# Kernel optimization log

Hardware: AMD Instinct MI355X
Metric: run time of the kernel (lower is better)

Reference implementation:

```python
import jax, jax.numpy as jnp
import numpy as np

B, N, C = 8, 8192, 256
H, D, S = 8, 32, 32          # heads, dim_head, slice_num
HID = 4 * C                  # mlp hidden


def layernorm(x, w, b, eps=1e-5):
    mu = jnp.mean(x, axis=-1, keepdims=True)
    var = jnp.mean(jnp.square(x - mu), axis=-1, keepdims=True)
    return (x - mu) * jax.lax.rsqrt(var + eps) * w + b


def setup_inputs() -> dict:
    key = jax.random.key(0)
    ks = jax.random.split(key, 16)
    s = lambda fan: 1.0 / np.sqrt(fan)
    return {
        "fx": jax.random.normal(ks[0], (B, N, C), jnp.float32),
        "ln1_w": jnp.ones((C,), jnp.float32),
        "ln1_b": jnp.zeros((C,), jnp.float32),
        "Wx": jax.random.uniform(ks[1], (C, C), jnp.float32, -s(C), s(C)),   # in_project_x weight [inner,dim]
        "bx": jax.random.uniform(ks[2], (C,), jnp.float32, -s(C), s(C)),
        "Wq": jax.random.uniform(ks[3], (S, D), jnp.float32, -s(D), s(D)),
        "Wk": jax.random.uniform(ks[4], (S, D), jnp.float32, -s(D), s(D)),
        "Wv": jax.random.uniform(ks[5], (D, D), jnp.float32, -s(D), s(D)),
        "Wo": jax.random.uniform(ks[6], (C, C), jnp.float32, -s(C), s(C)),   # to_out weight [dim,inner]
        "bo": jax.random.uniform(ks[7], (C,), jnp.float32, -s(C), s(C)),
        "ln2_w": jnp.ones((C,), jnp.float32),
        "ln2_b": jnp.zeros((C,), jnp.float32),
        "W1": jax.random.uniform(ks[8], (HID, C), jnp.float32, -s(C), s(C)),
        "b1": jax.random.uniform(ks[9], (HID,), jnp.float32, -s(C), s(C)),
        "W2": jax.random.uniform(ks[10], (C, HID), jnp.float32, -s(HID), s(HID)),
        "b2": jax.random.uniform(ks[11], (C,), jnp.float32, -s(HID), s(HID)),
    }


def linear_no_attn(x, Wx, bx, Wq, Wk, Wv, Wo, bo):
    # x: [B,N,C]
    x_mid = x @ Wx.T + bx                                   # [B,N,C]
    x_mid = x_mid.reshape(x.shape[0], x.shape[1], H, D).transpose(0, 2, 1, 3)  # [B,H,N,D]
    q = jax.nn.softmax(x_mid @ Wq.T, axis=-1)               # [B,H,N,S], softmax over slices
    k = jax.nn.softmax(x_mid @ Wk.T, axis=-2)               # [B,H,N,S], softmax over tokens
    v = x_mid @ Wv.T                                        # [B,H,N,D]
    kv = jnp.einsum('bhns,bhnd->bhsd', k, v)                # [B,H,S,D]
    qkv = jnp.einsum('bhns,bhsd->bhnd', q, kv)              # [B,H,N,D]
    qkv = qkv.transpose(0, 2, 1, 3).reshape(x.shape[0], x.shape[1], H * D)
    return qkv @ Wo.T + bo


def reference(fx, ln1_w, ln1_b, Wx, bx, Wq, Wk, Wv, Wo, bo, ln2_w, ln2_b, W1, b1, W2, b2):
    h = linear_no_attn(layernorm(fx, ln1_w, ln1_b), Wx, bx, Wq, Wk, Wv, Wo, bo) + fx
    y = layernorm(h, ln2_w, ln2_b)
    y = jax.nn.gelu(y @ W1.T + b1, approximate=False)       # MLP: pre + exact GELU, n_layers=0
    y = y @ W2.T + b2
    return y + h
```

## Files before the change

### kernel.cpp

```cpp
#include <hip/hip_runtime.h>
#include <math.h>


typedef __attribute__((ext_vector_type(8))) short bf8;
typedef __attribute__((ext_vector_type(4))) float f32x4;
typedef __attribute__((ext_vector_type(4))) unsigned short u16x4;
typedef __attribute__((ext_vector_type(8))) unsigned short u16x8;

__device__ __forceinline__ float b2f(unsigned short x) {
  union { unsigned u; float f; } t; t.u = ((unsigned)x) << 16; return t.f;
}
__device__ __forceinline__ unsigned short f2b(float f) {
  union { float f; unsigned u; } t; t.f = f;
  unsigned r = t.u + 0x7fffu + ((t.u >> 16) & 1u);
  return (unsigned short)(r >> 16);
}
__device__ __forceinline__ float gelu_exact(float x) {
  return 0.5f * x * (1.0f + erff(x * 0.7071067811865475f));
}
__device__ __forceinline__ float erf_fast(float x) {
  float ax = fabsf(x);
  float t = __builtin_amdgcn_rcpf(fmaf(0.3275911f, ax, 1.0f));
  float p = t * fmaf(t, fmaf(t, fmaf(t, fmaf(t, 1.061405429f, -1.453152027f),
                                     1.421413741f), -0.284496736f), 0.254829592f);
  float r = 1.0f - p * __expf(-ax * ax);
  return copysignf(r, x);
}
__device__ __forceinline__ float gelu_fast(float x) {
  return 0.5f * x * (1.0f + erf_fast(x * 0.7071067811865475f));
}

typedef __attribute__((address_space(1))) const void gas_void;
typedef __attribute__((address_space(3))) void las_void;
__device__ __forceinline__ void gl_lds16(const void* g, void* l) {
  __builtin_amdgcn_global_load_lds((gas_void*)g, (las_void*)l, 16, 0, 0);
}

__global__ void sniff_kernel(const unsigned* __restrict__ fx, int* __restrict__ flag,
                             unsigned* __restrict__ gate) {
  if (threadIdx.x == 0) {
    int cnt = 0;
    for (int i = 0; i < 64; i++) {
      unsigned e = (fx[i] >> 7) & 0xFFu;
      cnt += (e >= 117u && e <= 130u) ? 1 : 0;
    }
    *flag = (cnt >= 32) ? 1 : 0;
    *gate = 0u;
  }
}

struct CvtDesc { const void* src[15]; int off[15]; int n[15]; };

__global__ __launch_bounds__(256) void cvt_tab(CvtDesc d, unsigned short* __restrict__ wtab,
                                               const int* __restrict__ flagp) {
  const int seg = blockIdx.y;
  const int i = blockIdx.x * 256 + threadIdx.x;
  if (i >= d.n[seg]) return;
  unsigned short o;
  if (*flagp) o = ((const unsigned short*)d.src[seg])[i];
  else        o = f2b(((const float*)d.src[seg])[i]);
  wtab[d.off[seg] + i] = o;
}

__global__ __launch_bounds__(256) void build_big(
    const unsigned short* __restrict__ wq, const unsigned short* __restrict__ wk,
    unsigned short* __restrict__ Wqbig, unsigned short* __restrict__ Wkbig)
{
  const int idx = blockIdx.x * 256 + threadIdx.x;
  const int row = idx >> 8, col = idx & 255;
  const bool same = (row >> 5) == (col >> 5);
  const int wi = (row & 31) * 32 + (col & 31);
  Wqbig[idx] = same ? wq[wi] : (unsigned short)0;
  Wkbig[idx] = same ? wk[wi] : (unsigned short)0;
}

__global__ __launch_bounds__(256) void zero_u16(unsigned short* __restrict__ p, int n) {
  int i8 = (blockIdx.x * 256 + threadIdx.x) * 8;
  if (i8 < n) { u16x8 z = {}; *(u16x8*)&p[i8] = z; }
}

__global__ __launch_bounds__(256) void ln_stats(
    const void* __restrict__ X, const int* __restrict__ flagp, int amode,
    float* __restrict__ MU, float* __restrict__ RS)
{
  const int lane = threadIdx.x & 63;
  const int wave = threadIdx.x >> 6;
  const size_t row = (size_t)blockIdx.x * 4 + wave;
  const size_t base = row * 256 + lane * 4;
  const bool abf = amode ? ((*flagp) != 0) : true;
  float x0, x1, x2, x3;
  if (abf) {
    u16x4 uv = *(const u16x4*)&((const unsigned short*)X)[base];
    x0 = b2f(uv[0]); x1 = b2f(uv[1]); x2 = b2f(uv[2]); x3 = b2f(uv[3]);
  } else {
    f32x4 t = *(const f32x4*)&((const float*)X)[base];
    x0 = t[0]; x1 = t[1]; x2 = t[2]; x3 = t[3];
  }
  float s = x0 + x1 + x2 + x3;
  float q = x0*x0 + x1*x1 + x2*x2 + x3*x3;
  #pragma unroll
  for (int m = 1; m < 64; m <<= 1) { s += __shfl_xor(s, m, 64); q += __shfl_xor(q, m, 64); }
  float mean = s * (1.0f / 256.0f);
  float var  = q * (1.0f / 256.0f) - mean * mean;
  if (lane == 0) { MU[row] = mean; RS[row] = rsqrtf(var + 1e-5f); }
}

__global__ __launch_bounds__(256) void gemm_bt(
    const unsigned short* __restrict__ A,
    const unsigned short* __restrict__ W,
    const unsigned short* __restrict__ bias,
    const void* __restrict__ Res, const int* __restrict__ flagp,
    unsigned short* __restrict__ Y,
    int N, int K, int act, int mz, long wz)
{
  __shared__ __align__(16) unsigned short smem[3 * 8192];
  const int tid = threadIdx.x, lane = tid & 63, wave = tid >> 6;
  const size_t zrow = (size_t)blockIdx.z * mz;
  const int bm = blockIdx.x * 128, bn = blockIdx.y * 128;
  const int wm = (wave >> 1) * 64, wn = (wave & 1) * 64;
  const int quad = lane >> 4, l16 = lane & 15;
  const unsigned short* Wz = W + (size_t)blockIdx.z * wz;

  f32x4 acc[4][4] = {};
  const int r0 = tid >> 2;
  const int co = (tid & 3) * 8;
  const unsigned short* pa0 = &A[(zrow + bm + r0) * K + co];
  const unsigned short* pa1 = &A[(zrow + bm + r0 + 64) * K + co];
  const unsigned short* pb0 = &Wz[(size_t)(bn + r0) * K + co];
  const unsigned short* pb1 = &Wz[(size_t)(bn + r0 + 64) * K + co];
  const int nt = K >> 5;

  auto stage = [&](int t, int sl) {
    const int k0 = t << 5;
    unsigned short* b_ = &smem[sl * 8192 + tid * 8];
    gl_lds16(pa0 + k0, b_);
    gl_lds16(pa1 + k0, b_ + 2048);
    gl_lds16(pb0 + k0, b_ + 4096);
    gl_lds16(pb1 + k0, b_ + 6144);
  };

  stage(0, 0);
  if (nt > 1) stage(1, 1);
  int scur = 0, snew = 2;
  for (int t = 0; t < nt; ++t) {
    if (t + 2 < nt) {
      stage(t + 2, snew);
      asm volatile("s_waitcnt vmcnt(8)" ::: "memory");
    } else if (t + 1 < nt) {
      asm volatile("s_waitcnt vmcnt(4)" ::: "memory");
    } else {
      asm volatile("s_waitcnt vmcnt(0)" ::: "memory");
    }
    __builtin_amdgcn_s_barrier();
    __builtin_amdgcn_sched_barrier(0);

    const unsigned short* sa = &smem[scur * 8192];
    const unsigned short* sb = sa + 4096;
    bf8 af[4], bfr[4];
    #pragma unroll
    for (int i = 0; i < 4; i++) af[i]  = *(const bf8*)&sa[(wm + i * 16 + l16) * 32 + quad * 8];
    #pragma unroll
    for (int j = 0; j < 4; j++) bfr[j] = *(const bf8*)&sb[(wn + j * 16 + l16) * 32 + quad * 8];
    #pragma unroll
    for (int i = 0; i < 4; i++)
      #pragma unroll
      for (int j = 0; j < 4; j++)
        acc[i][j] = __builtin_amdgcn_mfma_f32_16x16x32_bf16(af[i], bfr[j], acc[i][j], 0, 0, 0);

    __builtin_amdgcn_sched_barrier(0);
    __builtin_amdgcn_s_barrier();
    scur = scur + 1 < 3 ? scur + 1 : 0;
    snew = snew + 1 < 3 ? snew + 1 : 0;
  }

  const bool rbf = Res ? ((*flagp) != 0) : true;
  float bv[4];
  #pragma unroll
  for (int j = 0; j < 4; j++) bv[j] = b2f(bias[bn + wn + j * 16 + l16]);
  #pragma unroll
  for (int i = 0; i < 4; i++)
    #pragma unroll
    for (int j = 0; j < 4; j++)
      #pragma unroll
      for (int r = 0; r < 4; r++) {
        float v = acc[i][j][r] + bv[j];
        if (act == 2) v = __expf(v);
        acc[i][j][r] = v;
      }
  if (act == 3) {
    #pragma unroll
    for (int i = 0; i < 4; i++)
      #pragma unroll
      for (int g = 0; g < 2; g++)
        #pragma unroll
        for (int r = 0; r < 4; r++) {
          float a0 = acc[i][2*g][r], a1 = acc[i][2*g+1][r];
          float m = fmaxf(a0, a1);
          #pragma unroll
          for (int msk = 1; msk < 16; msk <<= 1) m = fmaxf(m, __shfl_xor(m, msk, 64));
          float e0 = __expf(a0 - m), e1 = __expf(a1 - m);
          float s = e0 + e1;
          #pragma unroll
          for (int msk = 1; msk < 16; msk <<= 1) s += __shfl_xor(s, msk, 64);
          const float rz = 1.0f / s;
          acc[i][2*g][r] = e0 * rz; acc[i][2*g+1][r] = e1 * rz;
        }
  }

  float* cf = (float*)smem;
  const int whalf = wm >> 6;
  #pragma unroll
  for (int half = 0; half < 2; ++half) {
    __builtin_amdgcn_s_barrier();
    if (whalf == half) {
      #pragma unroll
      for (int i = 0; i < 4; i++)
        #pragma unroll
        for (int j = 0; j < 4; j++)
          #pragma unroll
          for (int r = 0; r < 4; r++)
            cf[(i * 16 + quad * 4 + r) * 132 + wn + j * 16 + l16] = acc[i][j][r];
    }
    __builtin_amdgcn_s_barrier();
    #pragma unroll
    for (int st = 0; st < 4; ++st) {
      const int e = st * 2048 + tid * 8;
      const int row = e >> 7;
      const int col = e & 127;
      const size_t gbase = (zrow + bm + half * 64 + row) * (size_t)N + bn + col;
      float v[8];
      #pragma unroll
      for (int u = 0; u < 8; u++) v[u] = cf[row * 132 + col + u];
      if (Res) {
        if (rbf) {
          u16x8 rv = *(const u16x8*)&((const unsigned short*)Res)[gbase];
          #pragma unroll
          for (int u = 0; u < 8; u++) v[u] += b2f(rv[u]);
        } else {
          f32x4 ra = *(const f32x4*)&((const float*)Res)[gbase];
          f32x4 rb = *(const f32x4*)&((const float*)Res)[gbase + 4];
          v[0] += ra[0]; v[1] += ra[1]; v[2] += ra[2]; v[3] += ra[3];
          v[4] += rb[0]; v[5] += rb[1]; v[6] += rb[2]; v[7] += rb[3];
        }
      }
      u16x8 o;
      #pragma unroll
      for (int u = 0; u < 8; u++) o[u] = f2b(v[u]);
      *(u16x8*)&Y[gbase] = o;
    }
  }
}

__global__ __launch_bounds__(256) void gemm_bt_ln(
    const void* __restrict__ A, const int* __restrict__ flagp, int amode,
    const float* __restrict__ MU, const float* __restrict__ RS,
    const unsigned short* __restrict__ lw, const unsigned short* __restrict__ lb,
    const unsigned short* __restrict__ W, const unsigned short* __restrict__ bias,
    unsigned short* __restrict__ Y, int N, int K, int act)
{
  __shared__ __align__(16) unsigned char smemc[32768];
  unsigned short* lA = (unsigned short*)smemc;
  unsigned short* lB = lA + 4096;
  const int tid = threadIdx.x, lane = tid & 63, wave = tid >> 6;
  const int bm = blockIdx.x * 128, bn = blockIdx.y * 128;
  const int wm = (wave >> 1) * 64, wn = (wave & 1) * 64;
  const int quad = lane >> 4, l16 = lane & 15;
  const bool abf = amode ? ((*flagp) != 0) : true;
  const unsigned short* Ab = (const unsigned short*)A;
  const float* Af = (const float*)A;

  f32x4 acc[4][4] = {};
  const int r0 = tid >> 2;
  const int co = (tid & 3) * 8;
  const unsigned short* pb0 = &W[(size_t)(bn + r0) * K + co];
  const unsigned short* pb1 = &W[(size_t)(bn + r0 + 64) * K + co];

  for (int k0 = 0; k0 < K; k0 += 32) {
    u16x8 wv8 = *(const u16x8*)&lw[k0 + co];
    u16x8 bv8 = *(const u16x8*)&lb[k0 + co];
    __syncthreads();
    gl_lds16(pb0 + k0, &lB[tid * 8]);
    gl_lds16(pb1 + k0, &lB[2048 + tid * 8]);
    #pragma unroll
    for (int half = 0; half < 2; half++) {
      const int ar = bm + r0 + half * 64;
      const float m_ = MU[ar], r_ = RS[ar];
      float xv[8];
      if (abf) {
        u16x8 t = *(const u16x8*)&Ab[(size_t)ar * K + k0 + co];
        #pragma unroll
        for (int e = 0; e < 8; e++) xv[e] = b2f(t[e]);
      } else {
        f32x4 t0 = *(const f32x4*)&Af[(size_t)ar * K + k0 + co];
        f32x4 t1 = *(const f32x4*)&Af[(size_t)ar * K + k0 + co + 4];
        xv[0]=t0[0]; xv[1]=t0[1]; xv[2]=t0[2]; xv[3]=t0[3];
        xv[4]=t1[0]; xv[5]=t1[1]; xv[6]=t1[2]; xv[7]=t1[3];
      }
      u16x8 o;
      #pragma unroll
      for (int e = 0; e < 8; e++)
        o[e] = f2b((xv[e] - m_) * r_ * b2f(wv8[e]) + b2f(bv8[e]));
      *(u16x8*)&lA[half * 2048 + tid * 8] = o;
    }
    __syncthreads();

    bf8 af[4], bfr[4];
    #pragma unroll
    for (int i = 0; i < 4; i++) af[i]  = *(const bf8*)&lA[(wm + i * 16 + l16) * 32 + quad * 8];
    #pragma unroll
    for (int j = 0; j < 4; j++) bfr[j] = *(const bf8*)&lB[(wn + j * 16 + l16) * 32 + quad * 8];
    #pragma unroll
    for (int i = 0; i < 4; i++)
      #pragma unroll
      for (int j = 0; j < 4; j++)
        acc[i][j] = __builtin_amdgcn_mfma_f32_16x16x32_bf16(af[i], bfr[j], acc[i][j], 0, 0, 0);
  }

  float bv[4];
  #pragma unroll
  for (int j = 0; j < 4; j++) bv[j] = b2f(bias[bn + wn + j * 16 + l16]);
  #pragma unroll
  for (int i = 0; i < 4; i++)
    #pragma unroll
    for (int j = 0; j < 4; j++)
      #pragma unroll
      for (int r = 0; r < 4; r++) {
        float v = acc[i][j][r] + bv[j];
        if (act) v = gelu_exact(v);
        acc[i][j][r] = v;
      }

  float* cf = (float*)smemc;
  const int whalf = wm >> 6;
  #pragma unroll
  for (int half = 0; half < 2; ++half) {
    __syncthreads();
    if (whalf == half) {
      #pragma unroll
      for (int i = 0; i < 4; i++)
        #pragma unroll
        for (int j = 0; j < 4; j++)
          #pragma unroll
          for (int r = 0; r < 4; r++)
            cf[(i * 16 + quad * 4 + r) * 128 + wn + j * 16 + l16] = acc[i][j][r];
    }
    __syncthreads();
    #pragma unroll
    for (int st = 0; st < 4; ++st) {
      const int e = st * 2048 + tid * 8;
      const int row = e >> 7;
      const size_t gbase = (size_t)(bm + half * 64 + row) * N + bn + (e & 127);
      u16x8 o;
      #pragma unroll
      for (int u = 0; u < 8; u++) o[u] = f2b(cf[e + u]);
      *(u16x8*)&Y[gbase] = o;
    }
  }
}

__global__ __launch_bounds__(256, 2) void fused_mlp(
    const unsigned short* __restrict__ Hlo,
    const unsigned short* __restrict__ Hhi,
    const float* __restrict__ MU, const float* __restrict__ RS,
    const unsigned short* __restrict__ lw, const unsigned short* __restrict__ lb,
    const unsigned short* __restrict__ W1, const unsigned short* __restrict__ bs1,
    const unsigned short* __restrict__ W2, const unsigned short* __restrict__ bs2,
    void* __restrict__ OUT, const int* __restrict__ flagp,
    unsigned* __restrict__ gate)
{
  __shared__ __align__(16) unsigned char smem[77824];
  const int tid = threadIdx.x, lane = tid & 63, wave = tid >> 6;
  const int quad = lane >> 4, l16 = lane & 15;
  const int bid = blockIdx.x;
  const bool low = (bid & 1) == 0;
  const long grow = (low ? 0L : 32768L) + (long)(bid >> 1) * 128;
  const unsigned short* hbase = low ? (Hlo + (size_t)grow * 256)
                                    : (Hhi + ((size_t)grow - 32768) * 256);

  auto stageW1 = [&](int c, int b) {
    const unsigned short* src = W1 + (size_t)c * 8192;
    unsigned char* dst = smem + b * 16384;
    #pragma unroll
    for (int s = 0; s < 4; s++) {
      const int unit = s * 256 + tid;
      const int row = unit >> 5, u = unit & 31;
      gl_lds16(src + row * 256 + ((u ^ (row & 7)) * 8), dst + unit * 16);
    }
  };
  auto stageW2 = [&](int c, int b) {
    const unsigned short* src = W2 + c * 32;
    unsigned char* dst = smem + 32768 + b * 16384;
    #pragma unroll
    for (int s = 0; s < 4; s++) {
      const int unit = s * 256 + tid;
      const int row = unit >> 2, u = unit & 3;
      gl_lds16(src + (size_t)row * 1024 + ((u ^ ((row >> 1) & 3)) * 8), dst + unit * 16);
    }
  };

  stageW1(0, 0);
  stageW2(0, 0);

  unsigned short* b1l = (unsigned short*)(smem + 75776);
  if (tid < 128) *(u16x8*)&b1l[tid * 8] = *(const u16x8*)&bs1[tid * 8];

  bf8 areg[2][8];
  #pragma unroll
  for (int rg = 0; rg < 2; rg++) {
    const int myrow = wave * 32 + rg * 16 + l16;
    const float m_ = MU[grow + myrow], r_ = RS[grow + myrow];
    const unsigned short* hr = hbase + (size_t)myrow * 256 + quad * 8;
    #pragma unroll
    for (int ks = 0; ks < 8; ks++) {
      u16x8 hv = *(const u16x8*)&hr[ks * 32];
      u16x8 wv = *(const u16x8*)&lw[ks * 32 + quad * 8];
      u16x8 bv = *(const u16x8*)&lb[ks * 32 + quad * 8];
      u16x8 o;
      #pragma unroll
      for (int e = 0; e < 8; e++)
        o[e] = f2b((b2f(hv[e]) - m_) * r_ * b2f(wv[e]) + b2f(bv[e]));
      *(u16x8*)&areg[rg][ks] = o;
    }
  }

  asm volatile("s_waitcnt vmcnt(0) lgkmcnt(0)" ::: "memory");
  __builtin_amdgcn_s_barrier();
  __builtin_amdgcn_sched_barrier(0);

  f32x4 acc[2][16] = {};
  unsigned short* tw = (unsigned short*)(smem + 65536 + wave * 2560);
  const int gsw = (l16 >> 1) & 3;
  int bsel = 0;

  for (int c = 0; c < 32; ++c) {
    if (c + 1 < 32) {
      stageW1(c + 1, bsel ^ 1);
      stageW2(c + 1, bsel ^ 1);
      __builtin_amdgcn_sched_barrier(0);
    }

    const unsigned short* w1b = (const unsigned short*)(smem + bsel * 16384);
    f32x4 p00 = {}, p01 = {}, p10 = {}, p11 = {};
    #pragma unroll
    for (int ks = 0; ks < 8; ks++) {
      const int slot = (ks * 4 + quad) ^ (l16 & 7);
      bf8 a0, a1;
      *(u16x8*)&a0 = *(const u16x8*)&w1b[l16 * 256 + slot * 8];
      *(u16x8*)&a1 = *(const u16x8*)&w1b[(16 + l16) * 256 + slot * 8];
      p00 = __builtin_amdgcn_mfma_f32_16x16x32_bf16(a0, areg[0][ks], p00, 0, 0, 0);
      p01 = __builtin_amdgcn_mfma_f32_16x16x32_bf16(a0, areg[1][ks], p01, 0, 0, 0);
      p10 = __builtin_amdgcn_mfma_f32_16x16x32_bf16(a1, areg[0][ks], p10, 0, 0, 0);
      p11 = __builtin_amdgcn_mfma_f32_16x16x32_bf16(a1, areg[1][ks], p11, 0, 0, 0);
    }

    {
      u16x4 bv0 = *(const u16x4*)&b1l[c * 32 + quad * 4];
      u16x4 bv1 = *(const u16x4*)&b1l[c * 32 + 16 + quad * 4];
      u16x4 o00, o01, o10, o11;
      #pragma unroll
      for (int r = 0; r < 4; r++) {
        o00[r] = f2b(gelu_fast(p00[r] + b2f(bv0[r])));
        o01[r] = f2b(gelu_fast(p01[r] + b2f(bv0[r])));
        o10[r] = f2b(gelu_fast(p10[r] + b2f(bv1[r])));
        o11[r] = f2b(gelu_fast(p11[r] + b2f(bv1[r])));
      }
      *(u16x4*)&tw[l16 * 40 + quad * 4]             = o00;
      *(u16x4*)&tw[(16 + l16) * 40 + quad * 4]      = o01;
      *(u16x4*)&tw[l16 * 40 + 16 + quad * 4]        = o10;
      *(u16x4*)&tw[(16 + l16) * 40 + 16 + quad * 4] = o11;
    }
    asm volatile("s_waitcnt lgkmcnt(0)" ::: "memory");
    __builtin_amdgcn_sched_barrier(0);

    bf8 ta0, ta1;
    *(u16x8*)&ta0 = *(const u16x8*)&tw[l16 * 40 + quad * 8];
    *(u16x8*)&ta1 = *(const u16x8*)&tw[(16 + l16) * 40 + quad * 8];
    const unsigned short* w2b = (const unsigned short*)(smem + 32768 + bsel * 16384);
    #pragma unroll
    for (int j = 0; j < 16; j++) {
      bf8 bw;
      *(u16x8*)&bw = *(const u16x8*)&w2b[(j * 16 + l16) * 32 + ((quad ^ gsw) * 8)];
      acc[0][j] = __builtin_amdgcn_mfma_f32_16x16x32_bf16(ta0, bw, acc[0][j], 0, 0, 0);
      acc[1][j] = __builtin_amdgcn_mfma_f32_16x16x32_bf16(ta1, bw, acc[1][j], 0, 0, 0);
    }

    asm volatile("s_waitcnt vmcnt(0)" ::: "memory");
    __builtin_amdgcn_s_barrier();
    __builtin_amdgcn_sched_barrier(0);
    bsel ^= 1;
  }

  if (!low) {
    if (tid == 0) {
      while (__hip_atomic_load(gate, __ATOMIC_ACQUIRE, __HIP_MEMORY_SCOPE_AGENT) < 256u)
        __builtin_amdgcn_s_sleep(32);
    }
    __syncthreads();
  }

  const bool obf = (*flagp) != 0;
  float* cf = (float*)smem;
  #pragma unroll
  for (int hh = 0; hh < 2; ++hh) {
    __syncthreads();
    if ((wave >> 1) == hh) {
      const int wl = (wave & 1) * 32;
      #pragma unroll
      for (int rg = 0; rg < 2; rg++)
        #pragma unroll
        for (int j = 0; j < 16; j++)
          #pragma unroll
          for (int r = 0; r < 4; r++)
            cf[(wl + rg * 16 + quad * 4 + r) * 260 + j * 16 + l16] = acc[rg][j][r];
    }
    __syncthreads();
    const unsigned short* hrow = hbase + (size_t)(hh * 64) * 256;
    #pragma unroll
    for (int s = 0; s < 8; s++) {
      const int e = s * 2048 + tid * 8;
      const int row = e >> 8, col = e & 255;
      u16x8 rv = *(const u16x8*)&hrow[e];
      u16x8 b2v = *(const u16x8*)&bs2[col];
      float v[8];
      #pragma unroll
      for (int u = 0; u < 8; u++) v[u] = cf[row * 260 + col + u] + b2f(rv[u]) + b2f(b2v[u]);
      const size_t ob = (size_t)(grow + hh * 64 + row) * 256 + col;
      if (obf) {
        u16x8 o;
        #pragma unroll
        for (int u = 0; u < 8; u++) o[u] = f2b(v[u]);
        *(u16x8*)&((unsigned short*)OUT)[ob] = o;
      } else {
        f32x4 oa, obv;
        oa[0]=v[0]; oa[1]=v[1]; oa[2]=v[2]; oa[3]=v[3];
        obv[0]=v[4]; obv[1]=v[5]; obv[2]=v[6]; obv[3]=v[7];
        *(f32x4*)&((float*)OUT)[ob] = oa;
        *(f32x4*)&((float*)OUT)[ob + 4] = obv;
      }
    }
  }

  if (low) {
    __syncthreads();
    if (tid == 0)
      __hip_atomic_fetch_add(gate, 1u, __ATOMIC_RELEASE, __HIP_MEMORY_SCOPE_AGENT);
  }
}

__global__ __launch_bounds__(256) void accumG(
    const unsigned short* __restrict__ X,
    const unsigned short* __restrict__ E,
    float* __restrict__ Gp)
{
  __shared__ float Xl[64 * 256];
  __shared__ __align__(16) unsigned short El[64 * 256];
  const int tid = threadIdx.x;
  const int k = blockIdx.x;
  const int h = tid >> 5, s = tid & 31;

  float acc[32];
  #pragma unroll
  for (int d = 0; d < 32; d++) acc[d] = 0.f;
  float zacc = 0.f;

  for (int sub = 0; sub < 4; sub++) {
    const size_t r0s = (size_t)k * 256 + sub * 64;
    __syncthreads();
    #pragma unroll
    for (int i = 0; i < 8; i++) {
      const int flat = i * 2048 + tid * 8;
      u16x8 xv = *(const u16x8*)&X[r0s * 256 + flat];
      #pragma unroll
      for (int e = 0; e < 8; e++) Xl[flat + e] = b2f(xv[e]);
      *(u16x8*)&El[flat] = *(const u16x8*)&E[r0s * 256 + flat];
    }
    __syncthreads();

    for (int t = 0; t < 64; t++) {
      const float e = b2f(El[t * 256 + h * 32 + s]);
      zacc += e;
      const int xb = t * 256 + h * 32;
      #pragma unroll
      for (int dq = 0; dq < 8; dq++) {
        f32x4 xv = *(const f32x4*)&Xl[xb + dq * 4];
        acc[dq*4+0] += e * xv[0];
        acc[dq*4+1] += e * xv[1];
        acc[dq*4+2] += e * xv[2];
        acc[dq*4+3] += e * xv[3];
      }
    }
  }

  float* gp = &Gp[(size_t)k * 8448 + (size_t)tid * 32];
  #pragma unroll
  for (int dq = 0; dq < 8; dq++) {
    f32x4 o; o[0]=acc[dq*4]; o[1]=acc[dq*4+1]; o[2]=acc[dq*4+2]; o[3]=acc[dq*4+3];
    *(f32x4*)&gp[dq * 4] = o;
  }
  Gp[(size_t)k * 8448 + 8192 + tid] = zacc;
}

__global__ __launch_bounds__(256) void reduceG(const float* __restrict__ Gp,
                                               float* __restrict__ Gfin) {
  const int o = blockIdx.x * 256 + threadIdx.x;
  if (o >= 67584) return;
  const int b = o / 8448;
  const int j = o - b * 8448;
  float s = 0.f;
  #pragma unroll 8
  for (int i = 0; i < 32; i++) s += Gp[(size_t)(b * 32 + i) * 8448 + j];
  Gfin[o] = s;
}

__global__ __launch_bounds__(256) void kv_build(
    const float* __restrict__ Gfin, const unsigned short* __restrict__ Wv,
    unsigned short* __restrict__ KVB)
{
  __shared__ float Gl[8192];
  __shared__ float zl[256];
  __shared__ float wvt[1024];
  const int tid = threadIdx.x;
  const int b = blockIdx.x;
  for (int i = tid; i < 8192; i += 256) Gl[i] = Gfin[(size_t)b * 8448 + i];
  zl[tid] = Gfin[(size_t)b * 8448 + 8192 + tid];
  for (int i = tid; i < 1024; i += 256) {
    const int dd = i >> 5, d = i & 31;
    wvt[i] = b2f(Wv[d * 32 + dd]);
  }
  __syncthreads();

  const int h = tid >> 5, d = tid & 31;
  unsigned short row[32];
  for (int s = 0; s < 32; s++) {
    float a = 0.f;
    #pragma unroll
    for (int dd = 0; dd < 32; dd++) a += Gl[h * 1024 + s * 32 + dd] * wvt[dd * 32 + d];
    row[s] = f2b(a / zl[h * 32 + s]);
  }
  unsigned short* out = &KVB[(size_t)b * 65536 + (size_t)(h * 32 + d) * 256 + h * 32];
  #pragma unroll
  for (int e = 0; e < 4; e++) *(u16x8*)&out[e * 8] = *(u16x8*)&row[e * 8];
}

__global__ __launch_bounds__(256) void copy_h0(const unsigned short* __restrict__ src,
                                               unsigned short* __restrict__ dst) {
  size_t i = ((size_t)blockIdx.x * 256 + threadIdx.x) * 8;
  *(u16x8*)&dst[i] = *(const u16x8*)&src[i];
}

extern "C" void kernel_launch(void* const* d_in, const int* in_sizes, int n_in,
                              void* d_out, int out_size, void* d_ws, size_t ws_size,
                              hipStream_t stream)
{
  const void* fx   = d_in[0];
  const void* ln1w = d_in[1];
  const void* ln1b = d_in[2];
  const void* Wx   = d_in[3];
  const void* bx   = d_in[4];
  const void* Wq   = d_in[5];
  const void* Wk   = d_in[6];
  const void* Wv   = d_in[7];
  const void* Wo   = d_in[8];
  const void* bo   = d_in[9];
  const void* ln2w = d_in[10];
  const void* ln2b = d_in[11];
  const void* W1   = d_in[12];
  const void* b1   = d_in[13];
  const void* W2   = d_in[14];
  const void* b2   = d_in[15];

  unsigned short* ws    = (unsigned short*)d_ws;
  unsigned short* hid   = ws;
  float* Gp             = (float*)ws;
  unsigned short* wtab  = ws + 8388608;
  unsigned short* h0res = wtab + 661248;
  float* Gfin           = (float*)h0res;
  unsigned short* Wqbig = h0res + 2097152;
  unsigned short* Wkbig = Wqbig + 65536;
  unsigned short* KVB   = Wkbig + 65536;
  unsigned short* zbias = KVB + 524288;
  float* fpw = (float*)(zbias + 256);
  float* mu1 = fpw;
  float* rs1 = fpw + 65536;
  float* mu2 = fpw + 131072;
  float* rs2 = fpw + 196608;
  int* flagp = (int*)(fpw + 262144);
  unsigned* gatep = (unsigned*)(flagp + 1);

  const int OFF_LN1W=0, OFF_LN1B=256, OFF_WX=512, OFF_BX=66048,
            OFF_WQ=66304, OFF_WK=67328, OFF_WV=68352,
            OFF_WO=69376, OFF_BO=134912, OFF_LN2W=135168, OFF_LN2B=135424,
            OFF_W1=135680, OFF_B1=397824, OFF_W2=398848, OFF_B2=660992;

  unsigned short* xm  = (unsigned short*)d_out;
  unsigned short* xup = xm + 16777216;

  sniff_kernel<<<1, 64, 0, stream>>>((const unsigned*)fx, flagp, gatep);
  CvtDesc cd;
  const void* srcs[15] = {ln1w, ln1b, Wx, bx, Wq, Wk, Wv, Wo, bo, ln2w, ln2b, W1, b1, W2, b2};
  const int offs[15]   = {OFF_LN1W, OFF_LN1B, OFF_WX, OFF_BX, OFF_WQ, OFF_WK, OFF_WV,
                          OFF_WO, OFF_BO, OFF_LN2W, OFF_LN2B, OFF_W1, OFF_B1, OFF_W2, OFF_B2};
  const int ns[15]     = {256, 256, 65536, 256, 1024, 1024, 1024, 65536, 256, 256, 256,
                          262144, 1024, 262144, 256};
  for (int i = 0; i < 15; i++) { cd.src[i] = srcs[i]; cd.off[i] = offs[i]; cd.n[i] = ns[i]; }
  cvt_tab<<<dim3(1024, 15), 256, 0, stream>>>(cd, wtab, flagp);
  build_big<<<256, 256, 0, stream>>>(wtab + OFF_WQ, wtab + OFF_WK, Wqbig, Wkbig);
  zero_u16<<<257, 256, 0, stream>>>(KVB, 524544);

  ln_stats<<<16384, 256, 0, stream>>>(fx, flagp, 1, mu1, rs1);
  gemm_bt_ln<<<dim3(512, 2), 256, 0, stream>>>(fx, flagp, 1, mu1, rs1,
      wtab + OFF_LN1W, wtab + OFF_LN1B, wtab + OFF_WX, wtab + OFF_BX,
      xm, 256, 256, 0);

  gemm_bt<<<dim3(512, 2), 256, 0, stream>>>(xm, Wkbig, zbias, nullptr, flagp,
                                            xup, 256, 256, 2, 0, 0);

  accumG<<<256, 256, 0, stream>>>(xm, xup, Gp);
  reduceG<<<264, 256, 0, stream>>>(Gp, Gfin);
  kv_build<<<8, 256, 0, stream>>>(Gfin, wtab + OFF_WV, KVB);

  gemm_bt<<<dim3(512, 2), 256, 0, stream>>>(xm, Wqbig, zbias, nullptr, flagp,
                                            xup, 256, 256, 3, 0, 0);

  gemm_bt<<<dim3(64, 2, 8), 256, 0, stream>>>(xup, KVB, zbias, nullptr, flagp,
                                              xm, 256, 256, 0, 8192, 65536);

  gemm_bt<<<dim3(512, 2), 256, 0, stream>>>(xm, wtab + OFF_WO, wtab + OFF_BO, fx, flagp,
                                            xup, 256, 256, 0, 0, 0);

  ln_stats<<<16384, 256, 0, stream>>>(xup, flagp, 0, mu2, rs2);
  copy_h0<<<4096, 256, 0, stream>>>(xup + (size_t)32768 * 256, hid);

  fused_mlp<<<512, 256, 0, stream>>>(xup, hid, mu2, rs2,
      wtab + OFF_LN2W, wtab + OFF_LN2B, wtab + OFF_W1, wtab + OFF_B1,
      wtab + OFF_W2, wtab + OFF_B2, d_out, flagp, gatep);
}
```

Measured before the change: 496.6 us.

## Double fused MLP block to 256 rows with 8 waves and software-pipelined W1 GEMM

The fused MLP kernel now uses 512 threads per block and handles 256 rows, so each staged W1/W2 chunk is shared across twice as many rows and the grid halves. W1 staging becomes triple-buffered two chunks ahead. The first GEMM for chunk c+1 is issued after the barrier, so it overlaps with the W2 load, and vmcnt waits are relaxed. LDS use grows to about 102 KB and the gate threshold is halved to match the block count, which may cut occupancy to one block per CU.

```diff
diff --git a/kernel.cpp b/kernel.cpp
--- a/kernel.cpp
+++ b/kernel.cpp
@@ -358,7 +358,7 @@
   }
 }
 
-__global__ __launch_bounds__(256, 2) void fused_mlp(
+__global__ __launch_bounds__(512, 2) void fused_mlp(
     const unsigned short* __restrict__ Hlo,
     const unsigned short* __restrict__ Hhi,
     const float* __restrict__ MU, const float* __restrict__ RS,
@@ -368,40 +368,37 @@
     void* __restrict__ OUT, const int* __restrict__ flagp,
     unsigned* __restrict__ gate)
 {
-  __shared__ __align__(16) unsigned char smem[77824];
+  __shared__ __align__(16) unsigned char smem[104448];
   const int tid = threadIdx.x, lane = tid & 63, wave = tid >> 6;
   const int quad = lane >> 4, l16 = lane & 15;
   const int bid = blockIdx.x;
   const bool low = (bid & 1) == 0;
-  const long grow = (low ? 0L : 32768L) + (long)(bid >> 1) * 128;
+  const long grow = (low ? 0L : 32768L) + (long)(bid >> 1) * 256;
   const unsigned short* hbase = low ? (Hlo + (size_t)grow * 256)
                                     : (Hhi + ((size_t)grow - 32768) * 256);
 
-  auto stageW1 = [&](int c, int b) {
+  auto stageW1 = [&](int c, int sl) {
     const unsigned short* src = W1 + (size_t)c * 8192;
-    unsigned char* dst = smem + b * 16384;
-    #pragma unroll
-    for (int s = 0; s < 4; s++) {
-      const int unit = s * 256 + tid;
+    unsigned char* dst = smem + sl * 16384;
+    #pragma unroll
+    for (int s = 0; s < 2; s++) {
+      const int unit = s * 512 + tid;
       const int row = unit >> 5, u = unit & 31;
       gl_lds16(src + row * 256 + ((u ^ (row & 7)) * 8), dst + unit * 16);
     }
   };
-  auto stageW2 = [&](int c, int b) {
+  auto stageW2 = [&](int c, int sl) {
     const unsigned short* src = W2 + c * 32;
-    unsigned char* dst = smem + 32768 + b * 16384;
-    #pragma unroll
-    for (int s = 0; s < 4; s++) {
-      const int unit = s * 256 + tid;
+    unsigned char* dst = smem + 49152 + sl * 16384;
+    #pragma unroll
+    for (int s = 0; s < 2; s++) {
+      const int unit = s * 512 + tid;
       const int row = unit >> 2, u = unit & 3;
       gl_lds16(src + (size_t)row * 1024 + ((u ^ ((row >> 1) & 3)) * 8), dst + unit * 16);
     }
   };
 
-  stageW1(0, 0);
-  stageW2(0, 0);
-
-  unsigned short* b1l = (unsigned short*)(smem + 75776);
+  unsigned short* b1l = (unsigned short*)(smem + 102400);
   if (tid < 128) *(u16x8*)&b1l[tid * 8] = *(const u16x8*)&bs1[tid * 8];
 
   bf8 areg[2][8];
@@ -422,25 +419,17 @@
       *(u16x8*)&areg[rg][ks] = o;
     }
   }
-
   asm volatile("s_waitcnt vmcnt(0) lgkmcnt(0)" ::: "memory");
+
+  stageW1(0, 0); stageW2(0, 0);
+  stageW1(1, 1); stageW2(1, 1);
+  asm volatile("s_waitcnt vmcnt(4)" ::: "memory");
   __builtin_amdgcn_s_barrier();
   __builtin_amdgcn_sched_barrier(0);
 
-  f32x4 acc[2][16] = {};
-  unsigned short* tw = (unsigned short*)(smem + 65536 + wave * 2560);
-  const int gsw = (l16 >> 1) & 3;
-  int bsel = 0;
-
-  for (int c = 0; c < 32; ++c) {
-    if (c + 1 < 32) {
-      stageW1(c + 1, bsel ^ 1);
-      stageW2(c + 1, bsel ^ 1);
-      __builtin_amdgcn_sched_barrier(0);
-    }
-
-    const unsigned short* w1b = (const unsigned short*)(smem + bsel * 16384);
-    f32x4 p00 = {}, p01 = {}, p10 = {}, p11 = {};
+  f32x4 p00 = {}, p01 = {}, p10 = {}, p11 = {};
+  {
+    const unsigned short* w1b = (const unsigned short*)smem;
     #pragma unroll
     for (int ks = 0; ks < 8; ks++) {
       const int slot = (ks * 4 + quad) ^ (l16 & 7);
@@ -452,6 +441,14 @@
       p10 = __builtin_amdgcn_mfma_f32_16x16x32_bf16(a1, areg[0][ks], p10, 0, 0, 0);
       p11 = __builtin_amdgcn_mfma_f32_16x16x32_bf16(a1, areg[1][ks], p11, 0, 0, 0);
     }
+  }
+
+  f32x4 acc[2][16] = {};
+  unsigned short* tw = (unsigned short*)(smem + 81920 + wave * 2560);
+  const int gsw = (l16 >> 1) & 3;
+
+  for (int c = 0; c < 32; ++c) {
+    if (c + 2 < 32) stageW1(c + 2, (c + 2) % 3);
 
     {
       u16x4 bv0 = *(const u16x4*)&b1l[c * 32 + quad * 4];
@@ -472,27 +469,46 @@
     asm volatile("s_waitcnt lgkmcnt(0)" ::: "memory");
     __builtin_amdgcn_sched_barrier(0);
 
-    bf8 ta0, ta1;
-    *(u16x8*)&ta0 = *(const u16x8*)&tw[l16 * 40 + quad * 8];
-    *(u16x8*)&ta1 = *(const u16x8*)&tw[(16 + l16) * 40 + quad * 8];
-    const unsigned short* w2b = (const unsigned short*)(smem + 32768 + bsel * 16384);
-    #pragma unroll
-    for (int j = 0; j < 16; j++) {
-      bf8 bw;
-      *(u16x8*)&bw = *(const u16x8*)&w2b[(j * 16 + l16) * 32 + ((quad ^ gsw) * 8)];
-      acc[0][j] = __builtin_amdgcn_mfma_f32_16x16x32_bf16(ta0, bw, acc[0][j], 0, 0, 0);
-      acc[1][j] = __builtin_amdgcn_mfma_f32_16x16x32_bf16(ta1, bw, acc[1][j], 0, 0, 0);
-    }
-
-    asm volatile("s_waitcnt vmcnt(0)" ::: "memory");
+    {
+      bf8 ta0, ta1;
+      *(u16x8*)&ta0 = *(const u16x8*)&tw[l16 * 40 + quad * 8];
+      *(u16x8*)&ta1 = *(const u16x8*)&tw[(16 + l16) * 40 + quad * 8];
+      const unsigned short* w2b = (const unsigned short*)(smem + 49152 + (c & 1) * 16384);
+      #pragma unroll
+      for (int j = 0; j < 16; j++) {
+        bf8 bw;
+        *(u16x8*)&bw = *(const u16x8*)&w2b[(j * 16 + l16) * 32 + ((quad ^ gsw) * 8)];
+        acc[0][j] = __builtin_amdgcn_mfma_f32_16x16x32_bf16(ta0, bw, acc[0][j], 0, 0, 0);
+        acc[1][j] = __builtin_amdgcn_mfma_f32_16x16x32_bf16(ta1, bw, acc[1][j], 0, 0, 0);
+      }
+    }
+
+    if (c + 2 < 32) asm volatile("s_waitcnt vmcnt(2)" ::: "memory");
+    else            asm volatile("s_waitcnt vmcnt(0)" ::: "memory");
     __builtin_amdgcn_s_barrier();
     __builtin_amdgcn_sched_barrier(0);
-    bsel ^= 1;
+
+    if (c + 2 < 32) stageW2(c + 2, (c + 2) & 1);
+    if (c + 1 < 32) {
+      const unsigned short* w1b = (const unsigned short*)(smem + ((c + 1) % 3) * 16384);
+      p00 = {}; p01 = {}; p10 = {}; p11 = {};
+      #pragma unroll
+      for (int ks = 0; ks < 8; ks++) {
+        const int slot = (ks * 4 + quad) ^ (l16 & 7);
+        bf8 a0, a1;
+        *(u16x8*)&a0 = *(const u16x8*)&w1b[l16 * 256 + slot * 8];
+        *(u16x8*)&a1 = *(const u16x8*)&w1b[(16 + l16) * 256 + slot * 8];
+        p00 = __builtin_amdgcn_mfma_f32_16x16x32_bf16(a0, areg[0][ks], p00, 0, 0, 0);
+        p01 = __builtin_amdgcn_mfma_f32_16x16x32_bf16(a0, areg[1][ks], p01, 0, 0, 0);
+        p10 = __builtin_amdgcn_mfma_f32_16x16x32_bf16(a1, areg[0][ks], p10, 0, 0, 0);
+        p11 = __builtin_amdgcn_mfma_f32_16x16x32_bf16(a1, areg[1][ks], p11, 0, 0, 0);
+      }
+    }
   }
 
   if (!low) {
     if (tid == 0) {
-      while (__hip_atomic_load(gate, __ATOMIC_ACQUIRE, __HIP_MEMORY_SCOPE_AGENT) < 256u)
+      while (__hip_atomic_load(gate, __ATOMIC_ACQUIRE, __HIP_MEMORY_SCOPE_AGENT) < 128u)
         __builtin_amdgcn_s_sleep(32);
     }
     __syncthreads();
@@ -501,9 +517,9 @@
   const bool obf = (*flagp) != 0;
   float* cf = (float*)smem;
   #pragma unroll
-  for (int hh = 0; hh < 2; ++hh) {
-    __syncthreads();
-    if ((wave >> 1) == hh) {
+  for (int q = 0; q < 4; ++q) {
+    __syncthreads();
+    if ((wave >> 1) == q) {
       const int wl = (wave & 1) * 32;
       #pragma unroll
       for (int rg = 0; rg < 2; rg++)
@@ -514,17 +530,17 @@
             cf[(wl + rg * 16 + quad * 4 + r) * 260 + j * 16 + l16] = acc[rg][j][r];
     }
     __syncthreads();
-    const unsigned short* hrow = hbase + (size_t)(hh * 64) * 256;
-    #pragma unroll
-    for (int s = 0; s < 8; s++) {
-      const int e = s * 2048 + tid * 8;
+    const unsigned short* hrow = hbase + (size_t)(q * 64) * 256;
+    #pragma unroll
+    for (int s = 0; s < 4; s++) {
+      const int e = s * 4096 + tid * 8;
       const int row = e >> 8, col = e & 255;
       u16x8 rv = *(const u16x8*)&hrow[e];
       u16x8 b2v = *(const u16x8*)&bs2[col];
       float v[8];
       #pragma unroll
       for (int u = 0; u < 8; u++) v[u] = cf[row * 260 + col + u] + b2f(rv[u]) + b2f(b2v[u]);
-      const size_t ob = (size_t)(grow + hh * 64 + row) * 256 + col;
+      const size_t ob = (size_t)(grow + q * 64 + row) * 256 + col;
       if (obf) {
         u16x8 o;
         #pragma unroll
@@ -731,7 +747,7 @@
   ln_stats<<<16384, 256, 0, stream>>>(xup, flagp, 0, mu2, rs2);
   copy_h0<<<4096, 256, 0, stream>>>(xup + (size_t)32768 * 256, hid);
 
-  fused_mlp<<<512, 256, 0, stream>>>(xup, hid, mu2, rs2,
+  fused_mlp<<<256, 512, 0, stream>>>(xup, hid, mu2, rs2,
       wtab + OFF_LN2W, wtab + OFF_LN2B, wtab + OFF_W1, wtab + OFF_B1,
       wtab + OFF_W2, wtab + OFF_B2, d_out, flagp, gatep);
 }
```

Measured after the change: 485.3 us. 1.02x faster.
